# Optimization experiments

Measured on AMD Instinct MI355X. Metric: run time of the kernel, lower is better.

Reference implementation:

```python
import jax, jax.numpy as jnp
import numpy as np

B, H, W, C = 8, 48, 48, 256
RADIUS = 6
EPS = 1e-5


def setup_inputs() -> dict:
    key = jax.random.key(0)
    ks = jax.random.split(key, 6)
    x = jax.random.normal(ks[0], (B, H, W, C), jnp.float32)
    corr = jax.random.normal(ks[1], (B, H, W, H, W), jnp.float32)
    # map: Linear(256,16), init N(0, sqrt(2/out_features)), zero bias
    map_w = jax.random.normal(ks[2], (16, C), jnp.float32) * np.sqrt(2.0 / 16)
    map_b = jnp.zeros((16,), jnp.float32)
    # meanMap: Linear(16,2) (zero-init in torch; use small random for nontrivial test)
    mean_w = jax.random.normal(ks[3], (2, 16), jnp.float32) * 0.01
    mean_b = jnp.zeros((2,), jnp.float32)
    # covMap: Linear(16,2), init N(0, sqrt(2/2))
    cov_w = jax.random.normal(ks[4], (2, 16), jnp.float32) * np.sqrt(2.0 / 2)
    cov_b = jnp.zeros((2,), jnp.float32)
    return dict(x=x, corr=corr, map_w=map_w, map_b=map_b,
                mean_w=mean_w, mean_b=mean_b, cov_w=cov_w, cov_b=cov_b)


def reference(x, corr, map_w, map_b, mean_w, mean_b, cov_w, cov_b):
    b, h, w, _ = x.shape
    # mapA = Linear(256,16) + Tanh
    tt = jnp.tanh(jnp.einsum('bhwc,oc->bhwo', x, map_w) + map_b)  # (b,h,w,16)
    mean_ofs = jnp.einsum('bhwo,po->bhwp', tt, mean_w) + mean_b   # (b,h,w,2)
    cv = (jnp.einsum('bhwo,po->bhwp', tt, cov_w) + cov_b).reshape(b, h * w, 2)
    # per_Corr_Normalization over dims [1,2] (per-batch scalar mean/std)
    mu = jnp.mean(cv, axis=(1, 2), keepdims=True)
    var = jnp.var(cv, axis=(1, 2), keepdims=True) + EPS
    cv = (cv - mu) / jnp.sqrt(var)
    cv = jax.nn.sigmoid(cv) * 5.0 + 0.05          # variances in [0.05, 5.05]
    det = cv[:, :, 0] * cv[:, :, 1]               # (b, h*w)
    cov = cv.reshape(b, h, w, 2)
    # base grid: coord[...,0]=x (col), coord[...,1]=y (row)
    coy, cox = jnp.meshgrid(jnp.arange(h, dtype=jnp.float32),
                            jnp.arange(w, dtype=jnp.float32), indexing='ij')
    coord = jnp.stack([cox, coy], axis=-1)        # (h,w,2)
    mean = coord + mean_ofs                       # (b,h,w,2)
    # radius-bounded Gaussian mask over correlation volume (b,h,w,h2,w2)
    xs = jnp.arange(w, dtype=jnp.float32)
    ys = jnp.arange(h, dtype=jnp.float32)
    dx = xs - mean[..., 0:1]                      # (b,h,w,w2)
    dy = ys - mean[..., 1:2]                      # (b,h,w,h2)
    qx = dx * dx / cov[..., 0:1]                  # (b,h,w,w2)
    qy = dy * dy / cov[..., 1:2]                  # (b,h,w,h2)
    inwin = (jnp.abs(dy) <= RADIUS)[..., :, None] & (jnp.abs(dx) <= RADIUS)[..., None, :]
    weight = jnp.exp(-0.5 * (qy[..., :, None] + qx[..., None, :])) * inwin  # (b,h,w,h2,w2)
    # custom CUDA op does not backprop into corr (grad None); residual path does
    masked = jax.lax.stop_gradient(corr) * weight
    denom = 6.28 * jnp.sqrt(det).reshape(b, h, w, 1, 1)
    corr1 = masked / denom + corr
    return corr1, mean, det
```

## Files before the change

kernel.cpp:

```cpp
#include <hip/hip_runtime.h>
#include <math.h>

#define Bn 8
#define Hn 48
#define Wn 48
#define Cn 256
#define HW (Hn*Wn)
#define PIX (Bn*HW)
#define RADF 6.0f
#define PPB 4

typedef float vfloat4 __attribute__((ext_vector_type(4)));

__global__ __launch_bounds__(256) void k1_mlp(
        const float* __restrict__ x,
        const float* __restrict__ map_w, const float* __restrict__ map_b,
        const float* __restrict__ mean_w, const float* __restrict__ mean_b,
        const float* __restrict__ cov_w,  const float* __restrict__ cov_b,
        float4* __restrict__ ws0, float* __restrict__ out_mean) {
    int tid = threadIdx.x;
    int o = tid & 15;
    int p = blockIdx.x * 16 + (tid >> 4);

    const float4* xr = (const float4*)(x + (size_t)p * Cn);
    const float4* wr = (const float4*)(map_w + (size_t)o * Cn);
    float acc = 0.f;
#pragma unroll 8
    for (int k = 0; k < Cn / 4; ++k) {
        float4 xv = xr[k], wv = wr[k];
        acc = fmaf(xv.x, wv.x, acc);
        acc = fmaf(xv.y, wv.y, acc);
        acc = fmaf(xv.z, wv.z, acc);
        acc = fmaf(xv.w, wv.w, acc);
    }
    float tt = tanhf(acc + map_b[o]);

    float m0 = tt * mean_w[o];
    float m1 = tt * mean_w[16 + o];
    float c0 = tt * cov_w[o];
    float c1 = tt * cov_w[16 + o];
#pragma unroll
    for (int off = 8; off; off >>= 1) {
        m0 += __shfl_xor(m0, off, 16);
        m1 += __shfl_xor(m1, off, 16);
        c0 += __shfl_xor(c0, off, 16);
        c1 += __shfl_xor(c1, off, 16);
    }
    if (o == 0) {
        int j = p % Wn;
        int i = (p / Wn) % Hn;
        float mx = m0 + mean_b[0] + (float)j;
        float my = m1 + mean_b[1] + (float)i;
        ws0[p] = make_float4(mx, my, c0 + cov_b[0], c1 + cov_b[1]);
        out_mean[(size_t)p * 2]     = mx;
        out_mean[(size_t)p * 2 + 1] = my;
    }
}

__global__ __launch_bounds__(256) void k2_norm(
        const float4* __restrict__ ws0,
        float4* __restrict__ ws2, float* __restrict__ out_det) {
    int b = blockIdx.x, tid = threadIdx.x;
    __shared__ float s1[256], s2[256];
    float sum = 0.f, sq = 0.f;
    for (int j = tid; j < HW; j += 256) {
        float4 r = ws0[b * HW + j];
        sum += r.z + r.w;
        sq = fmaf(r.z, r.z, sq);
        sq = fmaf(r.w, r.w, sq);
    }
    s1[tid] = sum; s2[tid] = sq;
    __syncthreads();
    for (int off = 128; off; off >>= 1) {
        if (tid < off) { s1[tid] += s1[tid + off]; s2[tid] += s2[tid + off]; }
        __syncthreads();
    }
    const float inv_n = 1.f / (2.f * HW);
    float mu   = s1[0] * inv_n;
    float var  = s2[0] * inv_n - mu * mu;
    float rstd = rsqrtf(var + 1e-5f);

    const float NL2E = -0.72134752044448169f;
    for (int j = tid; j < HW; j += 256) {
        float4 r = ws0[b * HW + j];
        float z0 = (r.z - mu) * rstd;
        float z1 = (r.w - mu) * rstd;
        float cv0 = 5.f / (1.f + __expf(-z0)) + 0.05f;
        float cv1 = 5.f / (1.f + __expf(-z1)) + 0.05f;
        float det = cv0 * cv1;
        out_det[b * HW + j] = det;
        float inv_denom = 1.f / (6.28f * sqrtf(det));
        ws2[b * HW + j] = make_float4(NL2E / cv0, NL2E / cv1, inv_denom, 0.f);
    }
}

__global__ __launch_bounds__(256) void k3_mask(
        const float* __restrict__ corr,
        const float4* __restrict__ ws0, const float4* __restrict__ ws2,
        float* __restrict__ out) {
    int bp = blockIdx.x * PPB;
    int tid = threadIdx.x;
    __shared__ float ex[PPB][Wn];
    __shared__ float ey[PPB][Hn];

    for (int e = tid; e < PPB * 96; e += 256) {
        int q = e / 96, r = e - q * 96;
        float4 m = ws0[bp + q];
        float4 c = ws2[bp + q];
        if (r < Wn) {
            float dx = (float)r - m.x;
            ex[q][r] = (fabsf(dx) <= RADF) ? exp2f(c.x * dx * dx) : 0.f;
        } else {
            int h2 = r - Wn;
            float dy = (float)h2 - m.y;
            ey[q][h2] = (fabsf(dy) <= RADF) ? exp2f(c.y * dy * dy) * c.z : 0.f;
        }
    }
    __syncthreads();

    const vfloat4* src = (const vfloat4*)(corr + (size_t)bp * HW);
    vfloat4*       dst = (vfloat4*)(out + (size_t)bp * HW);
#pragma unroll
    for (int it = 0; it < 9; ++it) {
        int i  = it * 256 + tid;
        int q  = i / 576;
        int r  = i - q * 576;
        int h2 = r / 12;
        int w2 = (r - h2 * 12) * 4;
        vfloat4 v = __builtin_nontemporal_load(&src[i]);
        float eyv = ey[q][h2];
        v.x = fmaf(v.x, eyv * ex[q][w2],     v.x);
        v.y = fmaf(v.y, eyv * ex[q][w2 + 1], v.y);
        v.z = fmaf(v.z, eyv * ex[q][w2 + 2], v.z);
        v.w = fmaf(v.w, eyv * ex[q][w2 + 3], v.w);
        __builtin_nontemporal_store(v, &dst[i]);
    }
}

extern "C" void kernel_launch(void* const* d_in, const int* in_sizes, int n_in,
                              void* d_out, int out_size, void* d_ws, size_t ws_size,
                              hipStream_t stream) {
    const float* x      = (const float*)d_in[0];
    const float* corr   = (const float*)d_in[1];
    const float* map_w  = (const float*)d_in[2];
    const float* map_b  = (const float*)d_in[3];
    const float* mean_w = (const float*)d_in[4];
    const float* mean_b = (const float*)d_in[5];
    const float* cov_w  = (const float*)d_in[6];
    const float* cov_b  = (const float*)d_in[7];

    float* out       = (float*)d_out;
    float* out_corr1 = out;
    float* out_mean  = out + (size_t)PIX * HW;
    float* out_det   = out_mean + (size_t)PIX * 2;

    float4* ws0 = (float4*)d_ws;
    float4* ws2 = ws0 + PIX;

    k1_mlp<<<PIX / 16, 256, 0, stream>>>(x, map_w, map_b, mean_w, mean_b,
                                         cov_w, cov_b, ws0, out_mean);
    k2_norm<<<Bn, 256, 0, stream>>>(ws0, ws2, out_det);
    k3_mask<<<PIX / PPB, 256, 0, stream>>>(corr, ws0, ws2, out_corr1);
}
```

Measured before the change: 347.4 us.

## Fuse per-batch normalization into MLP and mask kernels via atomic stats

Removes the separate normalization kernel. The MLP kernel now accumulates per-batch sum and sum-of-squares with block-level atomics, and the mask kernel computes the sigmoid variances, det and coefficients for its own pixels. A memset of the stats buffer is added, and the mask loop is reindexed so each wavefront handles one pixel. The aim is to drop a launch and a serialized 8-block kernel, in exchange for atomics and a memset.

```diff
diff --git a/kernel.cpp b/kernel.cpp
--- a/kernel.cpp
+++ b/kernel.cpp
@@ -17,7 +17,8 @@
         const float* __restrict__ map_w, const float* __restrict__ map_b,
         const float* __restrict__ mean_w, const float* __restrict__ mean_b,
         const float* __restrict__ cov_w,  const float* __restrict__ cov_b,
-        float4* __restrict__ ws0, float* __restrict__ out_mean) {
+        float4* __restrict__ ws0, float* __restrict__ out_mean,
+        float* __restrict__ stats) {
     int tid = threadIdx.x;
     int o = tid & 15;
     int p = blockIdx.x * 16 + (tid >> 4);
@@ -46,94 +47,99 @@
         c0 += __shfl_xor(c0, off, 16);
         c1 += __shfl_xor(c1, off, 16);
     }
+
+    __shared__ float ssum[16], ssq[16];
     if (o == 0) {
         int j = p % Wn;
         int i = (p / Wn) % Hn;
         float mx = m0 + mean_b[0] + (float)j;
         float my = m1 + mean_b[1] + (float)i;
-        ws0[p] = make_float4(mx, my, c0 + cov_b[0], c1 + cov_b[1]);
+        float cc0 = c0 + cov_b[0];
+        float cc1 = c1 + cov_b[1];
+        ws0[p] = make_float4(mx, my, cc0, cc1);
         out_mean[(size_t)p * 2]     = mx;
         out_mean[(size_t)p * 2 + 1] = my;
+        int slot = tid >> 4;
+        ssum[slot] = cc0 + cc1;
+        ssq[slot]  = fmaf(cc0, cc0, cc1 * cc1);
+    }
+    __syncthreads();
+    if (tid == 0) {
+        float s = 0.f, q = 0.f;
+#pragma unroll
+        for (int k = 0; k < 16; ++k) { s += ssum[k]; q += ssq[k]; }
+        int b = blockIdx.x / (HW / 16);
+        atomicAdd(&stats[b * 2],     s);
+        atomicAdd(&stats[b * 2 + 1], q);
     }
 }
 
-__global__ __launch_bounds__(256) void k2_norm(
+__global__ __launch_bounds__(256) void k3_mask(
+        const float* __restrict__ corr,
         const float4* __restrict__ ws0,
-        float4* __restrict__ ws2, float* __restrict__ out_det) {
-    int b = blockIdx.x, tid = threadIdx.x;
-    __shared__ float s1[256], s2[256];
-    float sum = 0.f, sq = 0.f;
-    for (int j = tid; j < HW; j += 256) {
-        float4 r = ws0[b * HW + j];
-        sum += r.z + r.w;
-        sq = fmaf(r.z, r.z, sq);
-        sq = fmaf(r.w, r.w, sq);
-    }
-    s1[tid] = sum; s2[tid] = sq;
-    __syncthreads();
-    for (int off = 128; off; off >>= 1) {
-        if (tid < off) { s1[tid] += s1[tid + off]; s2[tid] += s2[tid + off]; }
-        __syncthreads();
-    }
-    const float inv_n = 1.f / (2.f * HW);
-    float mu   = s1[0] * inv_n;
-    float var  = s2[0] * inv_n - mu * mu;
-    float rstd = rsqrtf(var + 1e-5f);
+        const float* __restrict__ stats,
+        float* __restrict__ out_det,
+        float* __restrict__ out) {
+    int bp = blockIdx.x * PPB;
+    int tid = threadIdx.x;
+    __shared__ float ex[PPB][Wn];
+    __shared__ float ey[PPB][Hn];
+    __shared__ float4 mm[PPB];
+    __shared__ float4 coef[PPB];
 
-    const float NL2E = -0.72134752044448169f;
-    for (int j = tid; j < HW; j += 256) {
-        float4 r = ws0[b * HW + j];
+    if (tid < PPB) {
+        int p = bp + tid;
+        int b = p / HW;
+        float4 r = ws0[p];
+        float sum = stats[b * 2], sq = stats[b * 2 + 1];
+        const float inv_n = 1.f / (2.f * HW);
+        float mu   = sum * inv_n;
+        float var  = sq * inv_n - mu * mu;
+        float rstd = rsqrtf(var + 1e-5f);
         float z0 = (r.z - mu) * rstd;
         float z1 = (r.w - mu) * rstd;
         float cv0 = 5.f / (1.f + __expf(-z0)) + 0.05f;
         float cv1 = 5.f / (1.f + __expf(-z1)) + 0.05f;
         float det = cv0 * cv1;
-        out_det[b * HW + j] = det;
-        float inv_denom = 1.f / (6.28f * sqrtf(det));
-        ws2[b * HW + j] = make_float4(NL2E / cv0, NL2E / cv1, inv_denom, 0.f);
+        out_det[p] = det;
+        const float NL2E = -0.72134752044448169f;
+        coef[tid] = make_float4(NL2E / cv0, NL2E / cv1,
+                                1.f / (6.28f * sqrtf(det)), 0.f);
+        mm[tid] = r;
     }
-}
-
-__global__ __launch_bounds__(256) void k3_mask(
-        const float* __restrict__ corr,
-        const float4* __restrict__ ws0, const float4* __restrict__ ws2,
-        float* __restrict__ out) {
-    int bp = blockIdx.x * PPB;
-    int tid = threadIdx.x;
-    __shared__ float ex[PPB][Wn];
-    __shared__ float ey[PPB][Hn];
+    __syncthreads();
 
     for (int e = tid; e < PPB * 96; e += 256) {
-        int q = e / 96, r = e - q * 96;
-        float4 m = ws0[bp + q];
-        float4 c = ws2[bp + q];
-        if (r < Wn) {
-            float dx = (float)r - m.x;
-            ex[q][r] = (fabsf(dx) <= RADF) ? exp2f(c.x * dx * dx) : 0.f;
+        int q = e / 96, rr = e - q * 96;
+        float4 m = mm[q];
+        float4 c = coef[q];
+        if (rr < Wn) {
+            float dx = (float)rr - m.x;
+            ex[q][rr] = (fabsf(dx) <= RADF) ? exp2f(c.x * dx * dx) : 0.f;
         } else {
-            int h2 = r - Wn;
+            int h2 = rr - Wn;
             float dy = (float)h2 - m.y;
             ey[q][h2] = (fabsf(dy) <= RADF) ? exp2f(c.y * dy * dy) * c.z : 0.f;
         }
     }
     __syncthreads();
 
-    const vfloat4* src = (const vfloat4*)(corr + (size_t)bp * HW);
-    vfloat4*       dst = (vfloat4*)(out + (size_t)bp * HW);
+    int q    = tid >> 6;
+    int lane = tid & 63;
+    const vfloat4* src = (const vfloat4*)(corr + (size_t)(bp + q) * HW);
+    vfloat4*       dst = (vfloat4*)(out + (size_t)(bp + q) * HW);
 #pragma unroll
     for (int it = 0; it < 9; ++it) {
-        int i  = it * 256 + tid;
-        int q  = i / 576;
-        int r  = i - q * 576;
+        int r  = it * 64 + lane;
         int h2 = r / 12;
         int w2 = (r - h2 * 12) * 4;
-        vfloat4 v = __builtin_nontemporal_load(&src[i]);
+        vfloat4 v = __builtin_nontemporal_load(&src[r]);
         float eyv = ey[q][h2];
         v.x = fmaf(v.x, eyv * ex[q][w2],     v.x);
         v.y = fmaf(v.y, eyv * ex[q][w2 + 1], v.y);
         v.z = fmaf(v.z, eyv * ex[q][w2 + 2], v.z);
         v.w = fmaf(v.w, eyv * ex[q][w2 + 3], v.w);
-        __builtin_nontemporal_store(v, &dst[i]);
+        __builtin_nontemporal_store(v, &dst[r]);
     }
 }
 
@@ -154,11 +160,12 @@
     float* out_mean  = out + (size_t)PIX * HW;
     float* out_det   = out_mean + (size_t)PIX * 2;
 
-    float4* ws0 = (float4*)d_ws;
-    float4* ws2 = ws0 + PIX;
+    float4* ws0   = (float4*)d_ws;
+    float*  stats = (float*)(ws0 + PIX);
+
+    hipMemsetAsync(stats, 0, Bn * 2 * sizeof(float), stream);
 
     k1_mlp<<<PIX / 16, 256, 0, stream>>>(x, map_w, map_b, mean_w, mean_b,
-                                         cov_w, cov_b, ws0, out_mean);
-    k2_norm<<<Bn, 256, 0, stream>>>(ws0, ws2, out_det);
-    k3_mask<<<PIX / PPB, 256, 0, stream>>>(corr, ws0, ws2, out_corr1);
+                                         cov_w, cov_b, ws0, out_mean, stats);
+    k3_mask<<<PIX / PPB, 256, 0, stream>>>(corr, ws0, stats, out_det, out_corr1);
 }
```

Result: no change. 349.3 us (+0.6%).
